# Optimization experiments

Hardware: AMD Instinct MI355X
Metric: run time of the kernel (lower is better)

Reference implementation:

```python
import jax, jax.numpy as jnp
import numpy as np

N = 100000; R2 = 500; H = 200; T = 3; E = 300000; R2E = 400000
SE = 4000; SR = 8; S2E = 8000
SLOPE = (1.0 / 8 + 1.0 / 3) / 2  # eval-mode F.rrelu negative slope


def l2norm(x):
    # F.normalize(x) along dim=1 with eps=1e-12
    return x / jnp.maximum(jnp.linalg.norm(x, axis=-1, keepdims=True), 1e-12)


def rrelu(x):
    return jnp.where(x >= 0, x, x * SLOPE)


def seg_mean(vals, seg, num):
    # mean of vals rows grouped by seg id; absent groups stay zero (matches x_input init)
    s = jax.ops.segment_sum(vals, seg, num_segments=num)
    c = jax.ops.segment_sum(jnp.ones((vals.shape[0],), vals.dtype), seg, num_segments=num)
    return s / jnp.maximum(c, 1.0)[:, None]


def lstm_cell(x, h, c, Wih, Whh, bih, bhh):
    g = x @ Wih.T + bih + h @ Whh.T + bhh
    i, f, gg, o = jnp.split(g, 4, axis=1)
    c2 = jax.nn.sigmoid(f) * c + jax.nn.sigmoid(i) * jnp.tanh(gg)
    return jax.nn.sigmoid(o) * jnp.tanh(c2), c2


def gru_cell(x, h, Wih, Whh, bih, bhh):
    gi = x @ Wih.T + bih
    gh = h @ Whh.T + bhh
    ir, iz, inn = jnp.split(gi, 3, axis=1)
    hr, hz, hn = jnp.split(gh, 3, axis=1)
    r = jax.nn.sigmoid(ir + hr)
    z = jax.nn.sigmoid(iz + hz)
    n = jnp.tanh(inn + r * hn)
    return (1 - z) * n + z * h


def rgcn_layer(h, rel_emb, src, dst, et, Wn, Wloop, Wevolve, num_nodes):
    # UnionRGCNLayer: msg = (h_src + rel_emb[etype]) @ W_neighbor, sum-aggregated at dst;
    # self loop uses evolve weight for nodes with in-edges, plain loop weight otherwise.
    msg = (h[src] + rel_emb[et]) @ Wn
    agg = jax.ops.segment_sum(msg, dst, num_segments=num_nodes)
    indeg = jax.ops.segment_sum(jnp.ones((src.shape[0],), h.dtype), dst, num_segments=num_nodes)
    loop = jnp.where((indeg > 0)[:, None], h @ Wevolve, h @ Wloop)
    return rrelu(agg + loop)


def setup_inputs() -> dict:
    key = jax.random.key(0)
    ks = iter(jax.random.split(key, 48))
    s = 1.0 / np.sqrt(H)
    d = {}
    d['src'] = jax.random.randint(next(ks), (T, E), 0, N)
    d['dst'] = jax.random.randint(next(ks), (T, E), 0, N)
    d['etype'] = jax.random.randint(next(ks), (T, E), 0, R2)
    d['r_to_e'] = jax.random.randint(next(ks), (T, R2E), 0, N)
    d['r_seg'] = jax.random.randint(next(ks), (T, R2E), 0, R2)
    d['s_src'] = jax.random.randint(next(ks), (T, SE), 0, R2)
    d['s_dst'] = jax.random.randint(next(ks), (T, SE), 0, R2)
    d['s_etype'] = jax.random.randint(next(ks), (T, SE), 0, SR)
    d['s_r_to_e'] = jax.random.randint(next(ks), (T, S2E), 0, R2)
    d['s_r_seg'] = jax.random.randint(next(ks), (T, S2E), 0, SR)
    d['dynamic_emb'] = jax.random.normal(next(ks), (N, H), jnp.float32)
    d['emb_rel'] = jax.random.normal(next(ks), (R2, H), jnp.float32) * s
    d['p_rel'] = jax.random.normal(next(ks), (SR, H), jnp.float32) * s
    d['Wih1'] = jax.random.normal(next(ks), (4 * H, 2 * H), jnp.float32) * s
    d['Whh1'] = jax.random.normal(next(ks), (4 * H, H), jnp.float32) * s
    d['bih1'] = jax.random.normal(next(ks), (4 * H,), jnp.float32) * s
    d['bhh1'] = jax.random.normal(next(ks), (4 * H,), jnp.float32) * s
    d['Wih2'] = jax.random.normal(next(ks), (4 * H, 2 * H), jnp.float32) * s
    d['Whh2'] = jax.random.normal(next(ks), (4 * H, H), jnp.float32) * s
    d['bih2'] = jax.random.normal(next(ks), (4 * H,), jnp.float32) * s
    d['bhh2'] = jax.random.normal(next(ks), (4 * H,), jnp.float32) * s
    d['Wih3'] = jax.random.normal(next(ks), (3 * H, H), jnp.float32) * s
    d['Whh3'] = jax.random.normal(next(ks), (3 * H, H), jnp.float32) * s
    d['bih3'] = jax.random.normal(next(ks), (3 * H,), jnp.float32) * s
    d['bhh3'] = jax.random.normal(next(ks), (3 * H,), jnp.float32) * s
    d['Wihe'] = jax.random.normal(next(ks), (3 * H, H), jnp.float32) * s
    d['Whhe'] = jax.random.normal(next(ks), (3 * H, H), jnp.float32) * s
    d['bihe'] = jax.random.normal(next(ks), (3 * H,), jnp.float32) * s
    d['bhhe'] = jax.random.normal(next(ks), (3 * H,), jnp.float32) * s
    for nm in ('Wn', 'Wl', 'We', 'sWn', 'sWl', 'sWe'):
        d[nm] = jax.random.normal(next(ks), (2, H, H), jnp.float32) * s
    return d


def reference(src, dst, etype, r_to_e, r_seg, s_src, s_dst, s_etype, s_r_to_e, s_r_seg,
              dynamic_emb, emb_rel, p_rel,
              Wih1, Whh1, bih1, bhh1, Wih2, Whh2, bih2, bhh2,
              Wih3, Whh3, bih3, bhh3, Wihe, Whhe, bihe, bhhe,
              Wn, Wl, We, sWn, sWl, sWe):
    h = l2norm(dynamic_emb)  # layer_norm=True path
    h_0 = c_0 = p_h_0 = p_c_0 = None
    history_embs = []
    rel_embs = []
    for t in range(T):
        # per-relation mean of involved entity embeddings (r_to_e grouped by uniq_r)
        x_input = seg_mean(h[r_to_e[t]], r_seg[t], R2)
        if t == 0:
            h_prev, c_prev = emb_rel, x_input
        else:
            h_prev, c_prev = h_0, c_0
        x_cat = jnp.concatenate([emb_rel, x_input], axis=1)
        h_0, c_0 = lstm_cell(x_cat, h_prev, c_prev, Wih1, Whh1, bih1, bhh1)
        h_0 = l2norm(h_0); c_0 = l2norm(c_0)
        # super-graph: per-super-relation mean of relation embeddings
        sx = seg_mean(h_0[s_r_to_e[t]], s_r_seg[t], SR)
        if t == 0:
            ph_prev, pc_prev = p_rel, sx
        else:
            ph_prev, pc_prev = p_h_0, p_c_0
        sx_cat = jnp.concatenate([p_rel, sx], axis=1)
        p_h_0, p_c_0 = lstm_cell(sx_cat, ph_prev, pc_prev, Wih2, Whh2, bih2, bhh2)
        p_h_0 = l2norm(p_h_0); p_c_0 = l2norm(p_c_0)
        # super RGCN over relation-nodes (2 UnionRGCN layers, same rel emb per layer)
        cur = h_0
        for l in range(2):
            cur = rgcn_layer(cur, p_h_0, s_src[t], s_dst[t], s_etype[t], sWn[l], sWl[l], sWe[l], R2)
        cur = l2norm(cur)
        h_0 = gru_cell(cur, h_0, Wih3, Whh3, bih3, bhh3)
        h_0 = l2norm(h_0)
        rel_embs.append(h_0)
        # entity RGCN over the snapshot graph
        cur_h = h
        for l in range(2):
            cur_h = rgcn_layer(cur_h, h_0, src[t], dst[t], etype[t], Wn[l], Wl[l], We[l], N)
        cur_h = l2norm(cur_h)
        h = gru_cell(cur_h, h, Wihe, Whhe, bihe, bhhe)
        h = l2norm(h)
        history_embs.append(h)
    return jnp.stack(history_embs), jnp.stack(rel_embs)
```

## Files before the change

kernel.cpp:

```cpp
#include <hip/hip_runtime.h>
#include <math.h>

#define N_NODES 100000
#define H 200
#define R2 500
#define T_STEPS 3
#define E_EDGES 300000
#define R2E 400000
#define SE_EDGES 4000
#define SR 8
#define S2E 8000
#define SLOPE 0.22916666666666666f
#define NB 64
#define RCHUNK ((R2E + NB - 1) / NB)
#define NCH 128
#define CHSZ ((N_NODES + NCH - 1) / NCH)
#define SPT  ((CHSZ + 255) / 256)

typedef unsigned short u16;
typedef unsigned int u32;
typedef __bf16 bf8 __attribute__((ext_vector_type(8)));
typedef float f32x4 __attribute__((ext_vector_type(4)));

static __device__ __forceinline__ float fsig(float x) { return 1.f / (1.f + __expf(-x)); }
static __device__ __forceinline__ float ftanh(float x) {
    float e = __expf(-2.f * fabsf(x));
    float t = (1.f - e) / (1.f + e);
    return (x >= 0.f) ? t : -t;
}
static __device__ __forceinline__ float bf2f(u32 lo16) {
    u32 v = lo16 << 16; float f; __builtin_memcpy(&f, &v, 4); return f;
}
static __device__ __forceinline__ u16 f2bf(float a) {
    __bf16 x = (__bf16)a; u16 u; __builtin_memcpy(&u, &x, 2); return u;
}
static __device__ __forceinline__ u32 pk2(float a, float b) {
    return (u32)f2bf(a) | ((u32)f2bf(b) << 16);
}
static __device__ __forceinline__ int xcd_swz(int b, int nwg) {
    int q = nwg >> 3, r = nwg & 7;
    int xcd = b & 7, u = b >> 3;
    int start = xcd * q + (xcd < r ? xcd : r);
    return start + u;
}

__global__ __launch_bounds__(256) void l2norm_k(const float* __restrict__ src, float* __restrict__ dst,
                                                u16* __restrict__ mir, int rows) {
    int wave = threadIdx.x >> 6, lane = threadIdx.x & 63;
    int r = blockIdx.x * 4 + wave;
    if (r >= rows) return;
    float4 v = make_float4(0.f, 0.f, 0.f, 0.f);
    if (lane < 50) v = *(const float4*)(src + (size_t)r * H + lane * 4);
    float s = v.x * v.x + v.y * v.y + v.z * v.z + v.w * v.w;
    for (int o = 32; o > 0; o >>= 1) s += __shfl_down(s, o);
    float rn = 1.f / fmaxf(sqrtf(__shfl(s, 0)), 1e-12f);
    if (lane < 50) {
        float4 o4 = make_float4(v.x * rn, v.y * rn, v.z * rn, v.w * rn);
        *(float4*)(dst + (size_t)r * H + lane * 4) = o4;
        if (mir) {
            uint2 u; u.x = pk2(o4.x, o4.y); u.y = pk2(o4.z, o4.w);
            *(uint2*)(mir + (size_t)r * H + lane * 4) = u;
        }
    }
}

__global__ __launch_bounds__(256) void l2norm_b_k(u16* __restrict__ buf, int rows) {
    int wave = threadIdx.x >> 6, lane = threadIdx.x & 63;
    int r = blockIdx.x * 4 + wave;
    if (r >= rows) return;
    uint2 u = make_uint2(0, 0);
    if (lane < 50) u = *(const uint2*)(buf + (size_t)r * H + lane * 4);
    float x0 = bf2f(u.x & 0xffff), x1 = bf2f(u.x >> 16);
    float x2 = bf2f(u.y & 0xffff), x3 = bf2f(u.y >> 16);
    float s = x0 * x0 + x1 * x1 + x2 * x2 + x3 * x3;
    for (int o = 32; o > 0; o >>= 1) s += __shfl_down(s, o);
    float rn = 1.f / fmaxf(sqrtf(__shfl(s, 0)), 1e-12f);
    if (lane < 50) {
        uint2 o2; o2.x = pk2(x0 * rn, x1 * rn); o2.y = pk2(x2 * rn, x3 * rn);
        *(uint2*)(buf + (size_t)r * H + lane * 4) = o2;
    }
}

__global__ __launch_bounds__(256) void l2norm_bb_k(const u16* __restrict__ src, float* __restrict__ dst,
                                                   u16* __restrict__ mir, int rows) {
    int wave = threadIdx.x >> 6, lane = threadIdx.x & 63;
    int r = blockIdx.x * 4 + wave;
    if (r >= rows) return;
    uint2 u = make_uint2(0, 0);
    if (lane < 50) u = *(const uint2*)(src + (size_t)r * H + lane * 4);
    float x0 = bf2f(u.x & 0xffff), x1 = bf2f(u.x >> 16);
    float x2 = bf2f(u.y & 0xffff), x3 = bf2f(u.y >> 16);
    float s = x0 * x0 + x1 * x1 + x2 * x2 + x3 * x3;
    for (int o = 32; o > 0; o >>= 1) s += __shfl_down(s, o);
    float rn = 1.f / fmaxf(sqrtf(__shfl(s, 0)), 1e-12f);
    if (lane < 50) {
        float4 o4 = make_float4(x0 * rn, x1 * rn, x2 * rn, x3 * rn);
        *(float4*)(dst + (size_t)r * H + lane * 4) = o4;
        uint2 o2; o2.x = pk2(o4.x, o4.y); o2.y = pk2(o4.z, o4.w);
        *(uint2*)(mir + (size_t)r * H + lane * 4) = o2;
    }
}

__global__ void wconv4_k(const float* __restrict__ W0, const float* __restrict__ W1,
                         const float* __restrict__ W2, const float* __restrict__ W3,
                         u16* __restrict__ o) {
    int m = blockIdx.y;
    const float* W = (m == 0) ? W0 : (m == 1) ? W1 : (m == 2) ? W2 : W3;
    int i = blockIdx.x * 256 + threadIdx.x;
    if (i < 40000) { int n = i / 200, k = i - n * 200; o[m * 40000 + i] = f2bf(W[k * 200 + n]); }
}
__global__ void wconv2_k(const float* __restrict__ Wa, const float* __restrict__ Wb, u16* __restrict__ o) {
    int i = blockIdx.x * 256 + threadIdx.x;
    if (i < 240000) o[i] = f2bf(i < 120000 ? Wa[i] : Wb[i - 120000]);
}

__global__ void cnt3_k(const int* __restrict__ d, int total, int per_t, int stride, int* __restrict__ cnt) {
    int i = blockIdx.x * 256 + threadIdx.x;
    if (i < total) { int t = i / per_t; atomicAdd(&cnt[t * stride + d[i]], 1); }
}

__global__ __launch_bounds__(256) void seg_cnt3_k(const int* __restrict__ seg, int per_t, int nseg,
                                                  int blocks_per_t, int* __restrict__ cnt) {
    __shared__ int lc[500];
    int t = blockIdx.x / blocks_per_t;
    int pb = blockIdx.x - t * blocks_per_t;
    const int* s = seg + (size_t)t * per_t;
    int* c = cnt + (size_t)t * nseg;
    for (int i = threadIdx.x; i < nseg; i += 256) lc[i] = 0;
    __syncthreads();
    int chunk = (per_t + blocks_per_t - 1) / blocks_per_t;
    int beg = pb * chunk;
    int end = beg + chunk; if (end > per_t) end = per_t;
    for (int i = beg + threadIdx.x; i < end; i += 256) atomicAdd(&lc[s[i]], 1);
    __syncthreads();
    for (int i = threadIdx.x; i < nseg; i += 256) if (lc[i]) atomicAdd(&c[i], lc[i]);
}

__global__ __launch_bounds__(256) void hist3_k(const int* __restrict__ seg,
                                               int* __restrict__ hist, int* __restrict__ cnt) {
    __shared__ int lc[R2];
    int t = blockIdx.x / NB;
    int pb = blockIdx.x - t * NB;
    const int* s = seg + (size_t)t * R2E;
    for (int i = threadIdx.x; i < R2; i += 256) lc[i] = 0;
    __syncthreads();
    int beg = pb * RCHUNK;
    int end = beg + RCHUNK; if (end > R2E) end = R2E;
    for (int i = beg + threadIdx.x; i < end; i += 256) atomicAdd(&lc[s[i]], 1);
    __syncthreads();
    int* hrow = hist + (size_t)(t * NB + pb) * R2;
    int* c = cnt + (size_t)t * R2;
    for (int i = threadIdx.x; i < R2; i += 256) {
        hrow[i] = lc[i];
        if (lc[i]) atomicAdd(&c[i], lc[i]);
    }
}

__global__ __launch_bounds__(1024) void scan3_k(const int* __restrict__ cntA, int* __restrict__ offA,
                                                int* __restrict__ curA, int n) {
    const int b = blockIdx.x;
    const int* cnt = cntA + (size_t)b * n;
    int* off = offA + (size_t)b * (n + 1);
    int* cur = curA + (size_t)b * n;
    __shared__ int part[1024];
    int tid = threadIdx.x;
    int per = (n + 1023) / 1024;
    int s0 = tid * per;
    int e0 = s0 + per; if (e0 > n) e0 = n;
    int sum = 0;
    for (int i = s0; i < e0; ++i) sum += cnt[i];
    part[tid] = sum;
    __syncthreads();
    for (int d = 1; d < 1024; d <<= 1) {
        int v = (tid >= d) ? part[tid - d] : 0;
        __syncthreads();
        part[tid] += v;
        __syncthreads();
    }
    int excl = (tid == 0) ? 0 : part[tid - 1];
    for (int i = s0; i < e0; ++i) { off[i] = excl; cur[i] = excl; excl += cnt[i]; }
    if (tid == 1023) off[n] = excl;
}

__global__ __launch_bounds__(256) void scanA_k(const int* __restrict__ cntA, int* __restrict__ bsum, int n) {
    int b = blockIdx.x;
    int t = b / NCH, ch = b - t * NCH;
    const int* cnt = cntA + (size_t)t * n;
    int base = ch * CHSZ;
    int cend = base + CHSZ; if (cend > n) cend = n;
    int s0 = base + threadIdx.x * SPT;
    int e0 = s0 + SPT; if (e0 > cend) e0 = cend;
    int sum = 0;
    for (int i = s0; i < e0 && i < cend; ++i) sum += cnt[i];
    __shared__ int red[256];
    red[threadIdx.x] = (s0 < cend) ? sum : 0;
    __syncthreads();
    for (int o = 128; o > 0; o >>= 1) {
        if (threadIdx.x < o) red[threadIdx.x] += red[threadIdx.x + o];
        __syncthreads();
    }
    if (threadIdx.x == 0) bsum[t * NCH + ch] = red[0];
}

__global__ __launch_bounds__(128) void scanB_k(const int* __restrict__ bsum, int* __restrict__ boff,
                                               int* __restrict__ offA, int n) {
    int t = blockIdx.x;
    int tid = threadIdx.x;
    __shared__ int part[128];
    int v = bsum[t * NCH + tid];
    part[tid] = v;
    __syncthreads();
    for (int d = 1; d < 128; d <<= 1) {
        int u = (tid >= d) ? part[tid - d] : 0;
        __syncthreads();
        part[tid] += u;
        __syncthreads();
    }
    boff[t * NCH + tid] = part[tid] - v;
    if (tid == 127) offA[(size_t)t * (n + 1) + n] = part[127];
}

__global__ __launch_bounds__(256) void scanC_k(const int* __restrict__ cntA, const int* __restrict__ boff,
                                               int* __restrict__ offA, int* __restrict__ curA, int n) {
    int b = blockIdx.x;
    int t = b / NCH, ch = b - t * NCH;
    const int* cnt = cntA + (size_t)t * n;
    int* off = offA + (size_t)t * (n + 1);
    int* cur = curA + (size_t)t * n;
    int base = ch * CHSZ;
    int cend = base + CHSZ; if (cend > n) cend = n;
    int s0 = base + threadIdx.x * SPT;
    int e0 = s0 + SPT; if (e0 > cend) e0 = cend;
    int sum = 0;
    for (int i = s0; i < e0 && i < cend; ++i) sum += cnt[i];
    __shared__ int part[256];
    int my = (s0 < cend) ? sum : 0;
    part[threadIdx.x] = my;
    __syncthreads();
    for (int d = 1; d < 256; d <<= 1) {
        int u = (threadIdx.x >= d) ? part[threadIdx.x - d] : 0;
        __syncthreads();
        part[threadIdx.x] += u;
        __syncthreads();
    }
    int excl = boff[t * NCH + ch] + part[threadIdx.x] - my;
    for (int i = s0; i < e0 && i < cend; ++i) {
        off[i] = excl; cur[i] = excl; excl += cnt[i];
    }
}

__global__ __launch_bounds__(64) void offs3_k(const int* __restrict__ hist, const int* __restrict__ csr,
                                              int* __restrict__ offb) {
    int b = blockIdx.x;
    int t = b / R2, s = b - t * R2;
    int lane = threadIdx.x;
    int v = hist[(size_t)(t * NB + lane) * R2 + s];
    int pre = v;
    for (int o = 1; o < 64; o <<= 1) {
        int u = __shfl_up(pre, o);
        if (lane >= o) pre += u;
    }
    int base = csr[(size_t)t * (R2 + 1) + s];
    offb[(size_t)(t * NB + lane) * R2 + s] = base + pre - v;
}

__global__ __launch_bounds__(256) void part3_k(const int* __restrict__ seg, const int* __restrict__ val,
                                               const int* __restrict__ offb, int* __restrict__ outp) {
    __shared__ int cur[R2];
    int t = blockIdx.x / NB;
    int pb = blockIdx.x - t * NB;
    const int* s = seg + (size_t)t * R2E;
    const int* v = val + (size_t)t * R2E;
    const int* ob = offb + (size_t)(t * NB + pb) * R2;
    int* o = outp + (size_t)t * R2E;
    for (int i = threadIdx.x; i < R2; i += 256) cur[i] = ob[i];
    __syncthreads();
    int beg = pb * RCHUNK;
    int end = beg + RCHUNK; if (end > R2E) end = R2E;
    for (int i = beg + threadIdx.x; i < end; i += 256) {
        int p = atomicAdd(&cur[s[i]], 1);
        o[p] = v[i];
    }
}

__global__ void scatter3_k(const int* __restrict__ dst, const int* __restrict__ src,
                           const int* __restrict__ et, int* __restrict__ cur,
                           int* __restrict__ psrc, int* __restrict__ pet,
                           int per_t, int stride, int total) {
    int i = blockIdx.x * 256 + threadIdx.x;
    if (i < total) {
        int t = i / per_t;
        int p = atomicAdd(&cur[t * stride + dst[i]], 1);
        psrc[(size_t)t * per_t + p] = src[i];
        pet[(size_t)t * per_t + p] = et[i];
    }
}

__global__ __launch_bounds__(256) void zlist3b_k(const int* __restrict__ cnt, int* __restrict__ zl,
                                                 int* __restrict__ nz, int n, int bpt) {
    int t = blockIdx.x / bpt;
    int pb = blockIdx.x - t * bpt;
    int i = pb * 256 + threadIdx.x;
    bool z = (i < n) && (cnt[(size_t)t * n + i] == 0);
    unsigned long long mask = __ballot(z);
    int wave = threadIdx.x >> 6, lane = threadIdx.x & 63;
    __shared__ int wbase[4];
    __shared__ int bbase;
    if (lane == 0) wbase[wave] = __popcll(mask);
    __syncthreads();
    if (threadIdx.x == 0) {
        int s0 = wbase[0], s1 = wbase[1], s2 = wbase[2], s3 = wbase[3];
        int tot = s0 + s1 + s2 + s3;
        bbase = tot ? atomicAdd(&nz[t], tot) : 0;
        wbase[0] = 0; wbase[1] = s0; wbase[2] = s0 + s1; wbase[3] = s0 + s1 + s2;
    }
    __syncthreads();
    if (z) {
        int off = bbase + wbase[wave] + __popcll(mask & ((1ull << lane) - 1ull));
        zl[(size_t)t * n + off] = i;
    }
}

#define SEG_CW 25
__global__ __launch_bounds__(256) void seg_acc_k(const float* __restrict__ hsrc,
                                                 const int* __restrict__ idx,
                                                 const int* __restrict__ seg, int n,
                                                 float* __restrict__ acc, int nseg) {
    __shared__ float lacc[500 * SEG_CW];
    int cg = blockIdx.x & 7;
    int pb = blockIdx.x >> 3;
    int NPB = gridDim.x >> 3;
    int t = threadIdx.x;
    for (int i = t; i < nseg * SEG_CW; i += 256) lacc[i] = 0.f;
    __syncthreads();
    int chunk = (n + NPB - 1) / NPB;
    int beg = pb * chunk;
    int end = beg + chunk; if (end > n) end = n;
    if (t < 250) {
        int il = t / SEG_CW;
        int c = t - il * SEG_CW;
        int col = cg * SEG_CW + c;
        for (int i = beg + il; i < end; i += 10) {
            int r = seg[i];
            int e = idx[i];
            atomicAdd(&lacc[r * SEG_CW + c], hsrc[(size_t)e * H + col]);
        }
    }
    __syncthreads();
    for (int i = t; i < nseg * SEG_CW; i += 256) {
        int r = i / SEG_CW, c = i - (i / SEG_CW) * SEG_CW;
        atomicAdd(&acc[(size_t)r * H + cg * SEG_CW + c], lacc[i]);
    }
}

__global__ void seg_div_k(float* __restrict__ acc, const int* __restrict__ cnt, int rows) {
    int i = blockIdx.x * blockDim.x + threadIdx.x;
    if (i < rows * H) {
        int c = cnt[i / H];
        acc[i] /= (float)(c > 0 ? c : 1);
    }
}

__global__ __launch_bounds__(256) void seg_mean_part_k(const u16* __restrict__ h,
                                                       const int* __restrict__ per,
                                                       const int* __restrict__ off,
                                                       float* __restrict__ xpart, int nseg) {
    int r = blockIdx.x >> 2;
    int p = blockIdx.x & 3;
    if (r >= nseg) return;
    int wv = threadIdx.x >> 6, lane = threadIdx.x & 63;
    int beg = off[r], end = off[r + 1];
    float a0 = 0.f, a1 = 0.f, a2 = 0.f, a3 = 0.f;
    for (int i = beg + p * 4 + wv; i < end; i += 16) {
        int e = per[i];
        if (lane < 50) {
            uint2 u = ((const uint2*)(h + (size_t)e * H))[lane];
            a0 += bf2f(u.x & 0xffff); a1 += bf2f(u.x >> 16);
            a2 += bf2f(u.y & 0xffff); a3 += bf2f(u.y >> 16);
        }
    }
    __shared__ float red[4][200];
    if (lane < 50) *(float4*)(&red[wv][lane * 4]) = make_float4(a0, a1, a2, a3);
    __syncthreads();
    int t = threadIdx.x;
    if (t < 200) {
        float s = red[0][t] + red[1][t] + red[2][t] + red[3][t];
        xpart[((size_t)p * nseg + r) * H + t] = s;
    }
}
__global__ void seg_fin_k(const float* __restrict__ xpart, const int* __restrict__ off,
                          float* __restrict__ acc, int nseg) {
    int i = blockIdx.x * 256 + threadIdx.x;
    if (i < nseg * H) {
        int r = i / H;
        size_t stride = (size_t)nseg * H;
        float s = xpart[i] + xpart[stride + i] + xpart[2 * stride + i] + xpart[3 * stride + i];
        int c = off[r + 1] - off[r];
        acc[i] = s / (float)(c > 0 ? c : 1);
    }
}

__global__ __launch_bounds__(256) void lstm_k(const float* __restrict__ x1, const float* __restrict__ x2,
                                              const float* __restrict__ hprev, const float* __restrict__ cprev,
                                              const float* __restrict__ Wih, const float* __restrict__ Whh,
                                              const float* __restrict__ bih, const float* __restrict__ bhh,
                                              float* __restrict__ hout, float* __restrict__ cout, int rows) {
    int r = blockIdx.x;
    if (r >= rows) return;
    __shared__ float xb[2 * H], hb[H], gb[4 * H], hv[H], cv[H];
    __shared__ float red[8];
    int t = threadIdx.x;
    for (int i = t; i < 2 * H; i += 256)
        xb[i] = (i < H) ? x1[(size_t)r * H + i] : x2[(size_t)r * H + i - H];
    if (t < H) hb[t] = hprev[(size_t)r * H + t];
    __syncthreads();
    for (int j = t; j < 4 * H; j += 256) {
        float s = bih[j] + bhh[j];
        const float* wi = Wih + (size_t)j * 2 * H;
        for (int k = 0; k < 2 * H; ++k) s += xb[k] * wi[k];
        const float* wh = Whh + (size_t)j * H;
        for (int k = 0; k < H; ++k) s += hb[k] * wh[k];
        gb[j] = s;
    }
    __syncthreads();
    if (t < H) {
        float ig = fsig(gb[t]);
        float fg = fsig(gb[H + t]);
        float gg = ftanh(gb[2 * H + t]);
        float og = fsig(gb[3 * H + t]);
        float c2 = fg * cprev[(size_t)r * H + t] + ig * gg;
        cv[t] = c2;
        hv[t] = og * ftanh(c2);
    }
    __syncthreads();
    float sh = 0.f, sc = 0.f;
    if (t < H) { sh = hv[t] * hv[t]; sc = cv[t] * cv[t]; }
    for (int o = 32; o > 0; o >>= 1) { sh += __shfl_down(sh, o); sc += __shfl_down(sc, o); }
    if ((t & 63) == 0) { red[t >> 6] = sh; red[4 + (t >> 6)] = sc; }
    __syncthreads();
    if (t == 0) {
        red[0] = 1.f / fmaxf(sqrtf(red[0] + red[1] + red[2] + red[3]), 1e-12f);
        red[4] = 1.f / fmaxf(sqrtf(red[4] + red[5] + red[6] + red[7]), 1e-12f);
    }
    __syncthreads();
    if (t < H) {
        hout[(size_t)r * H + t] = hv[t] * red[0];
        cout[(size_t)r * H + t] = cv[t] * red[4];
    }
}

__global__ __launch_bounds__(256) void gru_small_k(const float* __restrict__ x, const float* __restrict__ h,
                                                   const float* __restrict__ Wih, const float* __restrict__ Whh,
                                                   const float* __restrict__ bih, const float* __restrict__ bhh,
                                                   float* __restrict__ outp, u16* __restrict__ mirp, int rows) {
    int r = blockIdx.x;
    if (r >= rows) return;
    __shared__ float xb[H], hb[H], gi[3 * H], gh[3 * H], ov[H];
    __shared__ float red[4];
    int t = threadIdx.x;
    if (t < H) { xb[t] = x[(size_t)r * H + t]; hb[t] = h[(size_t)r * H + t]; }
    __syncthreads();
    for (int j = t; j < 3 * H; j += 256) {
        float si = bih[j], sh2 = bhh[j];
        const float* wi = Wih + (size_t)j * H;
        const float* wh = Whh + (size_t)j * H;
        for (int k = 0; k < H; ++k) { si += xb[k] * wi[k]; sh2 += hb[k] * wh[k]; }
        gi[j] = si; gh[j] = sh2;
    }
    __syncthreads();
    if (t < H) {
        float rr = fsig(gi[t] + gh[t]);
        float zz = fsig(gi[H + t] + gh[H + t]);
        float nn = ftanh(gi[2 * H + t] + rr * gh[2 * H + t]);
        ov[t] = (1.f - zz) * nn + zz * hb[t];
    }
    __syncthreads();
    float s = (t < H) ? ov[t] * ov[t] : 0.f;
    for (int o = 32; o > 0; o >>= 1) s += __shfl_down(s, o);
    if ((t & 63) == 0) red[t >> 6] = s;
    __syncthreads();
    if (t == 0) red[0] = 1.f / fmaxf(sqrtf(red[0] + red[1] + red[2] + red[3]), 1e-12f);
    __syncthreads();
    if (t < H) {
        float v = ov[t] * red[0];
        outp[(size_t)r * H + t] = v;
        mirp[(size_t)r * H + t] = f2bf(v);
    }
}

__global__ __launch_bounds__(256) void sup_fused_k(const float* __restrict__ cur, const float* __restrict__ prel,
                                                   const int* __restrict__ soff, const int* __restrict__ sssrc,
                                                   const int* __restrict__ sset,
                                                   const float* __restrict__ Wn, const float* __restrict__ We,
                                                   const float* __restrict__ Wl, const int* __restrict__ indeg,
                                                   float* __restrict__ outp) {
    int r = blockIdx.x;
    __shared__ float ar[H], cr[H];
    int t = threadIdx.x;
    if (t < H) {
        int beg = soff[r], end = soff[r + 1];
        float acc = 0.f;
        for (int i = beg; i < end; ++i)
            acc += cur[(size_t)sssrc[i] * H + t] + prel[(size_t)sset[i] * H + t];
        ar[t] = acc;
        cr[t] = cur[(size_t)r * H + t];
    }
    __syncthreads();
    const float* W2 = (indeg[r] > 0) ? We : Wl;
    if (t < H) {
        float s = 0.f;
        for (int k = 0; k < H; ++k) s += ar[k] * Wn[(size_t)k * H + t] + cr[k] * W2[(size_t)k * H + t];
        outp[(size_t)r * H + t] = (s >= 0.f) ? s : s * SLOPE;
    }
}

__global__ __launch_bounds__(256) void ent_agg_b_k(const u16* __restrict__ cur, const u16* __restrict__ rel,
                                                   const int* __restrict__ eoff, const int* __restrict__ esrc,
                                                   const int* __restrict__ eet, u16* __restrict__ agg, int n) {
    int wave = threadIdx.x >> 6, lane = threadIdx.x & 63;
    int v = blockIdx.x * 4 + wave;
    if (v >= n) return;
    float a0 = 0.f, a1 = 0.f, a2 = 0.f, a3 = 0.f;
    bool act = lane < 50;
    int beg = eoff[v], end = eoff[v + 1];
    int i = beg;
    for (; i + 2 <= end; i += 2) {
        int e0 = esrc[i], t0 = eet[i];
        int e1 = esrc[i + 1], t1 = eet[i + 1];
        if (act) {
            uint2 h0 = ((const uint2*)(cur + (size_t)e0 * H))[lane];
            uint2 h1 = ((const uint2*)(cur + (size_t)e1 * H))[lane];
            uint2 r0 = ((const uint2*)(rel + (size_t)t0 * H))[lane];
            uint2 r1 = ((const uint2*)(rel + (size_t)t1 * H))[lane];
            a0 += bf2f(h0.x & 0xffff) + bf2f(r0.x & 0xffff) + bf2f(h1.x & 0xffff) + bf2f(r1.x & 0xffff);
            a1 += bf2f(h0.x >> 16) + bf2f(r0.x >> 16) + bf2f(h1.x >> 16) + bf2f(r1.x >> 16);
            a2 += bf2f(h0.y & 0xffff) + bf2f(r0.y & 0xffff) + bf2f(h1.y & 0xffff) + bf2f(r1.y & 0xffff);
            a3 += bf2f(h0.y >> 16) + bf2f(r0.y >> 16) + bf2f(h1.y >> 16) + bf2f(r1.y >> 16);
        }
    }
    if (i < end) {
        int e0 = esrc[i], t0 = eet[i];
        if (act) {
            uint2 h0 = ((const uint2*)(cur + (size_t)e0 * H))[lane];
            uint2 r0 = ((const uint2*)(rel + (size_t)t0 * H))[lane];
            a0 += bf2f(h0.x & 0xffff) + bf2f(r0.x & 0xffff);
            a1 += bf2f(h0.x >> 16) + bf2f(r0.x >> 16);
            a2 += bf2f(h0.y & 0xffff) + bf2f(r0.y & 0xffff);
            a3 += bf2f(h0.y >> 16) + bf2f(r0.y >> 16);
        }
    }
    if (act) {
        uint2 o; o.x = pk2(a0, a1); o.y = pk2(a2, a3);
        ((uint2*)(agg + (size_t)v * H))[lane] = o;
    }
}

#define BSTR 108
__global__ __launch_bounds__(128) void gemm_bp_k(const u16* __restrict__ A1, const u16* __restrict__ A2,
                                                 const u16* __restrict__ B1, const u16* __restrict__ B2,
                                                 u16* __restrict__ Cm, int M, int Nc) {
    __shared__ __bf16 Bs[64 * BSTR];
    const int tid = threadIdx.x;
    int idx2 = xcd_swz(blockIdx.x, gridDim.x);
    const int m0 = (idx2 >> 2) * 128;
    const int n0 = (idx2 & 3) * 64;
    const int w = tid >> 6, lane = tid & 63;
    const int lr = lane & 15, lo = lane >> 4;
    const int mbase = m0 + w * 64;

    bf8 zb;
#pragma unroll
    for (int e = 0; e < 8; ++e) zb[e] = (__bf16)0.f;

    f32x4 acc[4][4];
#pragma unroll
    for (int i = 0; i < 4; ++i)
#pragma unroll
        for (int j = 0; j < 4; ++j)
#pragma unroll
            for (int e = 0; e < 4; ++e) acc[i][j][e] = 0.f;

    auto stageB = [&](const u16* Bp, int kbase, int nch) {
        for (int ch = tid; ch < 64 * nch; ch += 128) {
            int n = ch / nch, q = ch - n * nch;
            int ng = n0 + n;
            uint4 v = make_uint4(0, 0, 0, 0);
            if (ng < Nc) v = *(const uint4*)(Bp + (size_t)ng * 200 + kbase + q * 8);
            *(uint4*)(&Bs[n * BSTR + q * 8]) = v;
        }
    };
    auto loadA = [&](bf8* buf, const u16* Ap, int kt7) {
        int kk = kt7 * 32 + lo * 8;
        bool kv = kk < 200;
#pragma unroll
        for (int mf = 0; mf < 4; ++mf) {
            int m = mbase + mf * 16 + lr;
            bf8 v = zb;
            if (kv && m < M) v = *(const bf8*)(Ap + (size_t)m * 200 + kk);
            buf[mf] = v;
        }
    };
    auto mmaStep = [&](bf8* a, int kt7, int kbase) {
        int kk = kt7 * 32 + lo * 8;
        int kcl = (kk < 200) ? (kk - kbase) : 0;
#pragma unroll
        for (int nf = 0; nf < 4; ++nf) {
            bf8 b = *(const bf8*)(&Bs[(nf * 16 + lr) * BSTR + kcl]);
#pragma unroll
            for (int mf = 0; mf < 4; ++mf)
                acc[mf][nf] = __builtin_amdgcn_mfma_f32_16x16x32_bf16(a[mf], b, acc[mf][nf], 0, 0, 0);
        }
    };

    bf8 a0[4], a1[4];
    stageB(B1, 0, 12);
    __syncthreads();
    loadA(a0, A1, 0);
    loadA(a1, A1, 1); mmaStep(a0, 0, 0);
    loadA(a0, A1, 2); mmaStep(a1, 1, 0);
    loadA(a1, A1, 3); mmaStep(a0, 2, 0);
    __syncthreads();
    stageB(B1, 96, 13);
    __syncthreads();
    loadA(a0, A1, 4); mmaStep(a1, 3, 96);
    loadA(a1, A1, 5); mmaStep(a0, 4, 96);
    loadA(a0, A1, 6); mmaStep(a1, 5, 96);
    loadA(a1, A2, 0); mmaStep(a0, 6, 96);
    __syncthreads();
    stageB(B2, 0, 12);
    __syncthreads();
    loadA(a0, A2, 1); mmaStep(a1, 0, 0);
    loadA(a1, A2, 2); mmaStep(a0, 1, 0);
    loadA(a0, A2, 3); mmaStep(a1, 2, 0);
    __syncthreads();
    stageB(B2, 96, 13);
    __syncthreads();
    loadA(a1, A2, 4); mmaStep(a0, 3, 96);
    loadA(a0, A2, 5); mmaStep(a1, 4, 96);
    loadA(a1, A2, 6); mmaStep(a0, 5, 96);
    mmaStep(a1, 6, 96);

#pragma unroll
    for (int mf = 0; mf < 4; ++mf) {
#pragma unroll
        for (int r = 0; r < 4; ++r) {
            int m = mbase + mf * 16 + lo * 4 + r;
            if (m >= M) continue;
#pragma unroll
            for (int nf = 0; nf < 4; ++nf) {
                int n = n0 + nf * 16 + lr;
                if (n >= Nc) continue;
                float v = acc[mf][nf][r];
                v = (v >= 0.f) ? v : v * SLOPE;
                Cm[(size_t)m * Nc + n] = f2bf(v);
            }
        }
    }
}

__global__ __launch_bounds__(256) void fixup_b_k(const u16* __restrict__ h, const float* __restrict__ Wl,
                                                 const int* __restrict__ zl, const int* __restrict__ nz,
                                                 u16* __restrict__ outp) {
    __shared__ float xr[H];
    int nzv = *nz;
    for (int z = blockIdx.x; z < nzv; z += gridDim.x) {
        int row = zl[z];
        if (threadIdx.x < H) xr[threadIdx.x] = bf2f(h[(size_t)row * H + threadIdx.x]);
        __syncthreads();
        if (threadIdx.x < H) {
            float s = 0.f;
            for (int k = 0; k < H; ++k) s += xr[k] * Wl[(size_t)k * H + threadIdx.x];
            outp[(size_t)row * H + threadIdx.x] = f2bf((s >= 0.f) ? s : s * SLOPE);
        }
        __syncthreads();
    }
}

#define GCG2 13
#define GTPB 6
#define WSTR 204
__global__ __launch_bounds__(256, 4) void gru_wlds_k(const u16* __restrict__ Xb, const u16* __restrict__ Hb,
                                                     const u16* __restrict__ Wb,
                                                     const float* __restrict__ bih, const float* __restrict__ bhh,
                                                     u16* __restrict__ Outb, int M) {
    __shared__ __bf16 Ws[6][16 * WSTR];
    const int tid = threadIdx.x;
    int idx2 = xcd_swz(blockIdx.x, gridDim.x);
    const int cg = idx2 % GCG2;
    const int rb = idx2 / GCG2;
    const int w = tid >> 6, lane = tid & 63;
    const int lr = lane & 15, lo = lane >> 4;
    const int c0 = cg * 16;

    for (int ch = tid; ch < 2400; ch += 256) {
        int s = ch / 400;
        int rem = ch - s * 400;
        int col = rem / 25, q = rem - (rem / 25) * 25;
        int cc = c0 + col; if (cc > 199) cc = 199;
        uint4 v = *(const uint4*)(Wb + (size_t)(s * 200 + cc) * 200 + q * 8);
        *(uint4*)(&Ws[s][col * WSTR + q * 8]) = v;
    }
    __syncthreads();

    int c = c0 + lr;
    const bool cvalid = c < 200;
    const int cc = cvalid ? c : 199;
    const float b0 = bih[cc], b1 = bih[200 + cc], b2 = bih[400 + cc];
    const float b3 = bhh[cc], b4 = bhh[200 + cc], b5 = bhh[400 + cc];

    bf8 zb;
#pragma unroll
    for (int e = 0; e < 8; ++e) zb[e] = (__bf16)0.f;

    for (int tile = 0; tile < GTPB; ++tile) {
        int mbase = (rb * GTPB + tile) * 128 + w * 32;
        if (mbase >= M) break;
        int m0r = mbase + lr;      if (m0r >= M) m0r = M - 1;
        int m1r = mbase + 16 + lr; if (m1r >= M) m1r = M - 1;
        const u16* Xp0 = Xb + (size_t)m0r * 200 + lo * 8;
        const u16* Xp1 = Xb + (size_t)m1r * 200 + lo * 8;
        const u16* Hp0 = Hb + (size_t)m0r * 200 + lo * 8;
        const u16* Hp1 = Hb + (size_t)m1r * 200 + lo * 8;

        f32x4 acc[6][2];
#pragma unroll
        for (int s = 0; s < 6; ++s)
#pragma unroll
            for (int i = 0; i < 2; ++i)
#pragma unroll
                for (int e = 0; e < 4; ++e) acc[s][i][e] = 0.f;

#pragma unroll
        for (int kt = 0; kt < 7; ++kt) {
            const int koff = kt * 32;
            const bool kv = (kt < 6) || (lo == 0);
            const int kcl = kv ? (koff + lo * 8) : 0;
            bf8 xa0 = zb, xa1 = zb, ha0 = zb, ha1 = zb;
            if (kv) {
                xa0 = *(const bf8*)(Xp0 + koff);
                xa1 = *(const bf8*)(Xp1 + koff);
                ha0 = *(const bf8*)(Hp0 + koff);
                ha1 = *(const bf8*)(Hp1 + koff);
            }
#pragma unroll
            for (int s = 0; s < 6; ++s) {
                bf8 wv = *(const bf8*)(&Ws[s][lr * WSTR + kcl]);
                bf8 a0f = (s < 3) ? xa0 : ha0;
                bf8 a1f = (s < 3) ? xa1 : ha1;
                acc[s][0] = __builtin_amdgcn_mfma_f32_16x16x32_bf16(a0f, wv, acc[s][0], 0, 0, 0);
                acc[s][1] = __builtin_amdgcn_mfma_f32_16x16x32_bf16(a1f, wv, acc[s][1], 0, 0, 0);
            }
        }
        if (cvalid) {
#pragma unroll
            for (int mf = 0; mf < 2; ++mf) {
#pragma unroll
                for (int r = 0; r < 4; ++r) {
                    int m = mbase + mf * 16 + lo * 4 + r;
                    if (m >= M) continue;
                    float ir = acc[0][mf][r] + b0;
                    float iz = acc[1][mf][r] + b1;
                    float in_ = acc[2][mf][r] + b2;
                    float hr = acc[3][mf][r] + b3;
                    float hz = acc[4][mf][r] + b4;
                    float hn = acc[5][mf][r] + b5;
                    float rr = fsig(ir + hr);
                    float zz = fsig(iz + hz);
                    float nn = ftanh(in_ + rr * hn);
                    float hvv = bf2f(Hb[(size_t)m * 200 + c]);
                    Outb[(size_t)m * 200 + c] = f2bf((1.f - zz) * nn + zz * hvv);
                }
            }
        }
    }
}

extern "C" void kernel_launch(void* const* d_in, const int* in_sizes, int n_in,
                              void* d_out, int out_size, void* d_ws, size_t ws_size,
                              hipStream_t stream) {
    (void)in_sizes; (void)n_in; (void)out_size; (void)ws_size;
    const int* src  = (const int*)d_in[0];
    const int* dst  = (const int*)d_in[1];
    const int* etyp = (const int*)d_in[2];
    const int* rte  = (const int*)d_in[3];
    const int* rseg = (const int*)d_in[4];
    const int* ssrc = (const int*)d_in[5];
    const int* sdst = (const int*)d_in[6];
    const int* setp = (const int*)d_in[7];
    const int* srte = (const int*)d_in[8];
    const int* srseg= (const int*)d_in[9];
    const float* dyn     = (const float*)d_in[10];
    const float* emb_rel = (const float*)d_in[11];
    const float* p_rel   = (const float*)d_in[12];
    const float* Wih1 = (const float*)d_in[13]; const float* Whh1 = (const float*)d_in[14];
    const float* bih1 = (const float*)d_in[15]; const float* bhh1 = (const float*)d_in[16];
    const float* Wih2 = (const float*)d_in[17]; const float* Whh2 = (const float*)d_in[18];
    const float* bih2 = (const float*)d_in[19]; const float* bhh2 = (const float*)d_in[20];
    const float* Wih3 = (const float*)d_in[21]; const float* Whh3 = (const float*)d_in[22];
    const float* bih3 = (const float*)d_in[23]; const float* bhh3 = (const float*)d_in[24];
    const float* Wihe = (const float*)d_in[25]; const float* Whhe = (const float*)d_in[26];
    const float* bihe = (const float*)d_in[27]; const float* bhhe = (const float*)d_in[28];
    const float* Wn  = (const float*)d_in[29];
    const float* Wl  = (const float*)d_in[30];
    const float* We  = (const float*)d_in[31];
    const float* sWn = (const float*)d_in[32];
    const float* sWl = (const float*)d_in[33];
    const float* sWe = (const float*)d_in[34];

    float* out = (float*)d_out;
    const size_t NH = (size_t)N_NODES * H;
    float* relout = out + 3 * NH;

    char* wp = (char*)d_ws;
    auto carve = [&](size_t bytes) -> void* {
        void* p = (void*)wp;
        wp += (bytes + 255) & ~(size_t)255;
        return p;
    };
    u16* aggB = (u16*)carve(NH * 2);
    u16* m0b  = (u16*)carve(NH * 2);
    u16* m1b  = (u16*)carve(NH * 2);
    u16* hmir = (u16*)carve(NH * 2);
    u16* gob  = (u16*)carve(NH * 2);
    u16* relm = (u16*)carve((size_t)R2 * H * 2);
    u16* wtB  = (u16*)carve((size_t)400000 * 2);
    float* h0a  = (float*)carve((size_t)R2 * H * 4);
    float* c0b  = (float*)carve((size_t)R2 * H * 4);
    float* xin  = (float*)carve((size_t)R2 * H * 4);
    float* xpart= (float*)carve((size_t)4 * R2 * H * 4);
    float* srelA= (float*)carve((size_t)R2 * H * 4);
    float* srelB= (float*)carve((size_t)R2 * H * 4);
    float* sxin = (float*)carve((size_t)SR * H * 4);
    float* p_h  = (float*)carve((size_t)SR * H * 4);
    float* p_c  = (float*)carve((size_t)SR * H * 4);
    int* eoff3  = (int*)carve((size_t)3 * (N_NODES + 1) * 4);
    int* esrcp3 = (int*)carve((size_t)3 * E_EDGES * 4);
    int* eetp3  = (int*)carve((size_t)3 * E_EDGES * 4);
    int* zl3    = (int*)carve((size_t)3 * N_NODES * 4);
    int* nz3    = (int*)carve(3 * 4);
    int* rcsr3  = (int*)carve((size_t)3 * (R2 + 1) * 4);
    int* rper3  = (int*)carve((size_t)3 * R2E * 4);
    int* sindeg3= (int*)carve((size_t)3 * R2 * 4);
    int* scnt3  = (int*)carve((size_t)3 * SR * 4);
    int* hist3  = (int*)carve((size_t)3 * NB * R2 * 4);
    int* offb3  = (int*)carve((size_t)3 * NB * R2 * 4);
    int* soff3  = (int*)carve((size_t)3 * (R2 + 1) * 4);
    int* scur3  = (int*)carve((size_t)3 * R2 * 4);
    int* sssrc3 = (int*)carve((size_t)3 * SE_EDGES * 4);
    int* sset3  = (int*)carve((size_t)3 * SE_EDGES * 4);
    int* bsum3  = (int*)carve((size_t)3 * NCH * 4);
    int* boff3  = (int*)carve((size_t)3 * NCH * 4);
    int* ecnt3 = (int*)m0b;
    int* rcnt3 = (int*)m0b + 3 * N_NODES;
    int* ecur3 = (int*)aggB;
    int* rcur3 = (int*)aggB + 3 * N_NODES;

    dim3 wg4(157, 4);
    wconv4_k<<<wg4, 256, 0, stream>>>(Wn, We, Wn + 40000, We + 40000, wtB);
    wconv2_k<<<938, 256, 0, stream>>>(Wihe, Whhe, wtB + 160000);

    hipMemsetAsync(ecnt3, 0, (size_t)3 * N_NODES * 4, stream);
    hipMemsetAsync(rcnt3, 0, (size_t)3 * R2 * 4, stream);
    hipMemsetAsync(nz3, 0, 3 * 4, stream);
    hipMemsetAsync(sindeg3, 0, (size_t)3 * R2 * 4, stream);
    hipMemsetAsync(scnt3, 0, (size_t)3 * SR * 4, stream);
    cnt3_k<<<(3 * E_EDGES + 255) / 256, 256, 0, stream>>>(dst, 3 * E_EDGES, E_EDGES, N_NODES, ecnt3);
    scanA_k<<<3 * NCH, 256, 0, stream>>>(ecnt3, bsum3, N_NODES);
    scanB_k<<<3, 128, 0, stream>>>(bsum3, boff3, eoff3, N_NODES);
    scanC_k<<<3 * NCH, 256, 0, stream>>>(ecnt3, boff3, eoff3, ecur3, N_NODES);
    scatter3_k<<<(3 * E_EDGES + 255) / 256, 256, 0, stream>>>(dst, src, etyp, ecur3, esrcp3, eetp3,
                                                             E_EDGES, N_NODES, 3 * E_EDGES);
    {
        int bpt = (N_NODES + 255) / 256;
        zlist3b_k<<<3 * bpt, 256, 0, stream>>>(ecnt3, zl3, nz3, N_NODES, bpt);
    }
    hist3_k<<<3 * NB, 256, 0, stream>>>(rseg, hist3, rcnt3);
    scan3_k<<<3, 1024, 0, stream>>>(rcnt3, rcsr3, rcur3, R2);
    offs3_k<<<3 * R2, 64, 0, stream>>>(hist3, rcsr3, offb3);
    part3_k<<<3 * NB, 256, 0, stream>>>(rseg, rte, offb3, rper3);
    seg_cnt3_k<<<12, 256, 0, stream>>>(srseg, S2E, SR, 4, scnt3);
    cnt3_k<<<(3 * SE_EDGES + 255) / 256, 256, 0, stream>>>(sdst, 3 * SE_EDGES, SE_EDGES, R2, sindeg3);
    scan3_k<<<3, 1024, 0, stream>>>(sindeg3, soff3, scur3, R2);
    scatter3_k<<<(3 * SE_EDGES + 255) / 256, 256, 0, stream>>>(sdst, ssrc, setp, scur3, sssrc3, sset3,
                                                              SE_EDGES, R2, 3 * SE_EDGES);

    l2norm_k<<<(N_NODES + 3) / 4, 256, 0, stream>>>(dyn, out + NH, hmir, N_NODES);

    const int gw  = 4 * ((N_NODES + 127) / 128);
    const int NRB2 = (N_NODES + GTPB * 128 - 1) / (GTPB * 128);
    const int gwg = GCG2 * NRB2;

    for (int t = 0; t < T_STEPS; ++t) {
        const int* srte_t = srte + (size_t)t * S2E;
        const int* srseg_t= srseg + (size_t)t * S2E;
        const int* eoff_t = eoff3 + (size_t)t * (N_NODES + 1);
        const int* esrc_t = esrcp3 + (size_t)t * E_EDGES;
        const int* eet_t  = eetp3 + (size_t)t * E_EDGES;
        const int* zl_t   = zl3 + (size_t)t * N_NODES;
        const int* nz_t   = nz3 + t;
        const int* rcsr_t = rcsr3 + (size_t)t * (R2 + 1);
        const int* rper_t = rper3 + (size_t)t * R2E;
        const int* sind_t = sindeg3 + (size_t)t * R2;
        const int* scnt_t = scnt3 + (size_t)t * SR;
        const int* soff_t = soff3 + (size_t)t * (R2 + 1);
        const int* sssrc_t= sssrc3 + (size_t)t * SE_EDGES;
        const int* sset_t = sset3 + (size_t)t * SE_EDGES;

        float* hist = out + (size_t)t * NH;
        float* rel_t = relout + (size_t)t * R2 * H;
        const float* hprev = (t == 0) ? emb_rel : relout + (size_t)(t - 1) * R2 * H;
        const float* cprev = (t == 0) ? xin : c0b;
        const float* php   = (t == 0) ? p_rel : p_h;
        const float* pcp   = (t == 0) ? sxin : p_c;

        seg_mean_part_k<<<R2 * 4, 256, 0, stream>>>(hmir, rper_t, rcsr_t, xpart, R2);
        seg_fin_k<<<(R2 * H + 255) / 256, 256, 0, stream>>>(xpart, rcsr_t, xin, R2);
        lstm_k<<<R2, 256, 0, stream>>>(emb_rel, xin, hprev, cprev, Wih1, Whh1, bih1, bhh1, h0a, c0b, R2);
        hipMemsetAsync(sxin, 0, (size_t)SR * H * 4, stream);
        seg_acc_k<<<16 * 8, 256, 0, stream>>>(h0a, srte_t, srseg_t, S2E, sxin, SR);
        seg_div_k<<<(SR * H + 255) / 256, 256, 0, stream>>>(sxin, scnt_t, SR);
        lstm_k<<<SR, 256, 0, stream>>>(p_rel, sxin, php, pcp, Wih2, Whh2, bih2, bhh2, p_h, p_c, SR);
        sup_fused_k<<<R2, 256, 0, stream>>>(h0a, p_h, soff_t, sssrc_t, sset_t, sWn, sWe, sWl, sind_t, srelA);
        sup_fused_k<<<R2, 256, 0, stream>>>(srelA, p_h, soff_t, sssrc_t, sset_t,
                                            sWn + H * H, sWe + H * H, sWl + H * H, sind_t, srelB);
        l2norm_k<<<(R2 + 3) / 4, 256, 0, stream>>>(srelB, srelB, (u16*)nullptr, R2);
        gru_small_k<<<R2, 256, 0, stream>>>(srelB, h0a, Wih3, Whh3, bih3, bhh3, rel_t, relm, R2);

        ent_agg_b_k<<<(N_NODES + 3) / 4, 256, 0, stream>>>(hmir, relm, eoff_t, esrc_t, eet_t, aggB, N_NODES);
        gemm_bp_k<<<gw, 128, 0, stream>>>(aggB, hmir, wtB, wtB + 40000, m0b, N_NODES, H);
        fixup_b_k<<<2048, 256, 0, stream>>>(hmir, Wl, zl_t, nz_t, m0b);
        ent_agg_b_k<<<(N_NODES + 3) / 4, 256, 0, stream>>>(m0b, relm, eoff_t, esrc_t, eet_t, aggB, N_NODES);
        gemm_bp_k<<<gw, 128, 0, stream>>>(aggB, m0b, wtB + 80000, wtB + 120000, m1b, N_NODES, H);
        fixup_b_k<<<2048, 256, 0, stream>>>(m0b, Wl + H * H, zl_t, nz_t, m1b);
        l2norm_b_k<<<(N_NODES + 3) / 4, 256, 0, stream>>>(m1b, N_NODES);

        gru_wlds_k<<<gwg, 256, 0, stream>>>(m1b, hmir, wtB + 160000, bihe, bhhe, gob, N_NODES);
        l2norm_bb_k<<<(N_NODES + 3) / 4, 256, 0, stream>>>(gob, hist, hmir, N_NODES);
    }
}
```

Measured before the change: 2.641 ms.

## Fuse super-relation segment mean and skip empty GEMM column fragments

The super-relation segment mean (memset, atomic accumulate, divide, plus a precompute count kernel) is replaced by one kernel with one block per super-relation. Each block scans all 8000 entries, accumulates matching rows in shared memory and divides by a count it computes itself. Separately, the bf16 GEMM skips MFMA work and B staging for the last column tile, where only 8 of 64 columns are valid (H=200). This cuts wasted matrix work across the large entity GEMMs, at the cost of an extra branch in the inner loop and a serial scan of the segment list in each of 8 blocks.

```diff
diff --git a/kernel.cpp b/kernel.cpp
--- a/kernel.cpp
+++ b/kernel.cpp
@@ -119,23 +119,6 @@
     if (i < total) { int t = i / per_t; atomicAdd(&cnt[t * stride + d[i]], 1); }
 }
 
-__global__ __launch_bounds__(256) void seg_cnt3_k(const int* __restrict__ seg, int per_t, int nseg,
-                                                  int blocks_per_t, int* __restrict__ cnt) {
-    __shared__ int lc[500];
-    int t = blockIdx.x / blocks_per_t;
-    int pb = blockIdx.x - t * blocks_per_t;
-    const int* s = seg + (size_t)t * per_t;
-    int* c = cnt + (size_t)t * nseg;
-    for (int i = threadIdx.x; i < nseg; i += 256) lc[i] = 0;
-    __syncthreads();
-    int chunk = (per_t + blocks_per_t - 1) / blocks_per_t;
-    int beg = pb * chunk;
-    int end = beg + chunk; if (end > per_t) end = per_t;
-    for (int i = beg + threadIdx.x; i < end; i += 256) atomicAdd(&lc[s[i]], 1);
-    __syncthreads();
-    for (int i = threadIdx.x; i < nseg; i += 256) if (lc[i]) atomicAdd(&c[i], lc[i]);
-}
-
 __global__ __launch_bounds__(256) void hist3_k(const int* __restrict__ seg,
                                                int* __restrict__ hist, int* __restrict__ cnt) {
     __shared__ int lc[R2];
@@ -321,43 +304,36 @@
     }
 }
 
-#define SEG_CW 25
-__global__ __launch_bounds__(256) void seg_acc_k(const float* __restrict__ hsrc,
-                                                 const int* __restrict__ idx,
-                                                 const int* __restrict__ seg, int n,
-                                                 float* __restrict__ acc, int nseg) {
-    __shared__ float lacc[500 * SEG_CW];
-    int cg = blockIdx.x & 7;
-    int pb = blockIdx.x >> 3;
-    int NPB = gridDim.x >> 3;
+__global__ __launch_bounds__(256) void seg_mean_sr_k(const float* __restrict__ h,
+                                                     const int* __restrict__ idx,
+                                                     const int* __restrict__ seg,
+                                                     float* __restrict__ outp) {
+    int r = blockIdx.x;
+    int wv = threadIdx.x >> 6, lane = threadIdx.x & 63;
+    __shared__ float acc[4][200];
+    __shared__ int cntl[4];
+    for (int i = threadIdx.x; i < 800; i += 256) ((float*)acc)[i] = 0.f;
+    __syncthreads();
+    int cnt = 0;
+    for (int i = wv; i < S2E; i += 4) {
+        if (seg[i] == r) {
+            const float* row = h + (size_t)idx[i] * H;
+            acc[wv][lane] += row[lane];
+            acc[wv][lane + 64] += row[lane + 64];
+            int c3 = lane + 128;
+            acc[wv][c3] += row[c3];
+            int c4 = lane + 192;
+            if (c4 < 200) acc[wv][c4] += row[c4];
+            ++cnt;
+        }
+    }
+    if (lane == 0) cntl[wv] = cnt;
+    __syncthreads();
     int t = threadIdx.x;
-    for (int i = t; i < nseg * SEG_CW; i += 256) lacc[i] = 0.f;
-    __syncthreads();
-    int chunk = (n + NPB - 1) / NPB;
-    int beg = pb * chunk;
-    int end = beg + chunk; if (end > n) end = n;
-    if (t < 250) {
-        int il = t / SEG_CW;
-        int c = t - il * SEG_CW;
-        int col = cg * SEG_CW + c;
-        for (int i = beg + il; i < end; i += 10) {
-            int r = seg[i];
-            int e = idx[i];
-            atomicAdd(&lacc[r * SEG_CW + c], hsrc[(size_t)e * H + col]);
-        }
-    }
-    __syncthreads();
-    for (int i = t; i < nseg * SEG_CW; i += 256) {
-        int r = i / SEG_CW, c = i - (i / SEG_CW) * SEG_CW;
-        atomicAdd(&acc[(size_t)r * H + cg * SEG_CW + c], lacc[i]);
-    }
-}
-
-__global__ void seg_div_k(float* __restrict__ acc, const int* __restrict__ cnt, int rows) {
-    int i = blockIdx.x * blockDim.x + threadIdx.x;
-    if (i < rows * H) {
-        int c = cnt[i / H];
-        acc[i] /= (float)(c > 0 ? c : 1);
+    if (t < 200) {
+        float s = acc[0][t] + acc[1][t] + acc[2][t] + acc[3][t];
+        int c = cntl[0] + cntl[1] + cntl[2] + cntl[3];
+        outp[(size_t)r * H + t] = s / (float)(c > 0 ? c : 1);
     }
 }
 
@@ -564,6 +540,8 @@
     int idx2 = xcd_swz(blockIdx.x, gridDim.x);
     const int m0 = (idx2 >> 2) * 128;
     const int n0 = (idx2 & 3) * 64;
+    const int nfb = (n0 + 16 >= Nc) ? 1 : 4;
+    const int brows = (nfb == 1) ? 16 : 64;
     const int w = tid >> 6, lane = tid & 63;
     const int lr = lane & 15, lo = lane >> 4;
     const int mbase = m0 + w * 64;
@@ -581,7 +559,7 @@
             for (int e = 0; e < 4; ++e) acc[i][j][e] = 0.f;
 
     auto stageB = [&](const u16* Bp, int kbase, int nch) {
-        for (int ch = tid; ch < 64 * nch; ch += 128) {
+        for (int ch = tid; ch < brows * nch; ch += 128) {
             int n = ch / nch, q = ch - n * nch;
             int ng = n0 + n;
             uint4 v = make_uint4(0, 0, 0, 0);
@@ -605,10 +583,12 @@
         int kcl = (kk < 200) ? (kk - kbase) : 0;
 #pragma unroll
         for (int nf = 0; nf < 4; ++nf) {
-            bf8 b = *(const bf8*)(&Bs[(nf * 16 + lr) * BSTR + kcl]);
-#pragma unroll
-            for (int mf = 0; mf < 4; ++mf)
-                acc[mf][nf] = __builtin_amdgcn_mfma_f32_16x16x32_bf16(a[mf], b, acc[mf][nf], 0, 0, 0);
+            if (nf < nfb) {
+                bf8 b = *(const bf8*)(&Bs[(nf * 16 + lr) * BSTR + kcl]);
+#pragma unroll
+                for (int mf = 0; mf < 4; ++mf)
+                    acc[mf][nf] = __builtin_amdgcn_mfma_f32_16x16x32_bf16(a[mf], b, acc[mf][nf], 0, 0, 0);
+            }
         }
     };
 
@@ -648,6 +628,7 @@
             if (m >= M) continue;
 #pragma unroll
             for (int nf = 0; nf < 4; ++nf) {
+                if (nf >= nfb) continue;
                 int n = n0 + nf * 16 + lr;
                 if (n >= Nc) continue;
                 float v = acc[mf][nf][r];
@@ -841,7 +822,6 @@
     int* rcsr3  = (int*)carve((size_t)3 * (R2 + 1) * 4);
     int* rper3  = (int*)carve((size_t)3 * R2E * 4);
     int* sindeg3= (int*)carve((size_t)3 * R2 * 4);
-    int* scnt3  = (int*)carve((size_t)3 * SR * 4);
     int* hist3  = (int*)carve((size_t)3 * NB * R2 * 4);
     int* offb3  = (int*)carve((size_t)3 * NB * R2 * 4);
     int* soff3  = (int*)carve((size_t)3 * (R2 + 1) * 4);
@@ -863,7 +843,6 @@
     hipMemsetAsync(rcnt3, 0, (size_t)3 * R2 * 4, stream);
     hipMemsetAsync(nz3, 0, 3 * 4, stream);
     hipMemsetAsync(sindeg3, 0, (size_t)3 * R2 * 4, stream);
-    hipMemsetAsync(scnt3, 0, (size_t)3 * SR * 4, stream);
     cnt3_k<<<(3 * E_EDGES + 255) / 256, 256, 0, stream>>>(dst, 3 * E_EDGES, E_EDGES, N_NODES, ecnt3);
     scanA_k<<<3 * NCH, 256, 0, stream>>>(ecnt3, bsum3, N_NODES);
     scanB_k<<<3, 128, 0, stream>>>(bsum3, boff3, eoff3, N_NODES);
@@ -878,7 +857,6 @@
     scan3_k<<<3, 1024, 0, stream>>>(rcnt3, rcsr3, rcur3, R2);
     offs3_k<<<3 * R2, 64, 0, stream>>>(hist3, rcsr3, offb3);
     part3_k<<<3 * NB, 256, 0, stream>>>(rseg, rte, offb3, rper3);
-    seg_cnt3_k<<<12, 256, 0, stream>>>(srseg, S2E, SR, 4, scnt3);
     cnt3_k<<<(3 * SE_EDGES + 255) / 256, 256, 0, stream>>>(sdst, 3 * SE_EDGES, SE_EDGES, R2, sindeg3);
     scan3_k<<<3, 1024, 0, stream>>>(sindeg3, soff3, scur3, R2);
     scatter3_k<<<(3 * SE_EDGES + 255) / 256, 256, 0, stream>>>(sdst, ssrc, setp, scur3, sssrc3, sset3,
@@ -901,7 +879,6 @@
         const int* rcsr_t = rcsr3 + (size_t)t * (R2 + 1);
         const int* rper_t = rper3 + (size_t)t * R2E;
         const int* sind_t = sindeg3 + (size_t)t * R2;
-        const int* scnt_t = scnt3 + (size_t)t * SR;
         const int* soff_t = soff3 + (size_t)t * (R2 + 1);
         const int* sssrc_t= sssrc3 + (size_t)t * SE_EDGES;
         const int* sset_t = sset3 + (size_t)t * SE_EDGES;
@@ -916,9 +893,7 @@
         seg_mean_part_k<<<R2 * 4, 256, 0, stream>>>(hmir, rper_t, rcsr_t, xpart, R2);
         seg_fin_k<<<(R2 * H + 255) / 256, 256, 0, stream>>>(xpart, rcsr_t, xin, R2);
         lstm_k<<<R2, 256, 0, stream>>>(emb_rel, xin, hprev, cprev, Wih1, Whh1, bih1, bhh1, h0a, c0b, R2);
-        hipMemsetAsync(sxin, 0, (size_t)SR * H * 4, stream);
-        seg_acc_k<<<16 * 8, 256, 0, stream>>>(h0a, srte_t, srseg_t, S2E, sxin, SR);
-        seg_div_k<<<(SR * H + 255) / 256, 256, 0, stream>>>(sxin, scnt_t, SR);
+        seg_mean_sr_k<<<SR, 256, 0, stream>>>(h0a, srte_t, srseg_t, sxin);
         lstm_k<<<SR, 256, 0, stream>>>(p_rel, sxin, php, pcp, Wih2, Whh2, bih2, bhh2, p_h, p_c, SR);
         sup_fused_k<<<R2, 256, 0, stream>>>(h0a, p_h, soff_t, sssrc_t, sset_t, sWn, sWe, sWl, sind_t, srelA);
         sup_fused_k<<<R2, 256, 0, stream>>>(srelA, p_h, soff_t, sssrc_t, sset_t,
```

New measurement: 3.592 ms. 36.0% more time.
